# Kernel tuning notes

Measured on AMD Instinct MI355X. Metric: run time of the kernel, lower is better.

The kernel has to match this reference:

```python
import jax, jax.numpy as jnp
import numpy as np

H = 768          # hidden_size
NH = 12          # num_attention_heads
DH = H // NH     # attention_head_size = 64
NE_TYPES = 16    # num_edge_types
B, S = 4, 512
N = B * S        # flattened node count
E = 131072       # number of edges


def setup_inputs() -> dict:
    key = jax.random.key(0)
    ks = jax.random.split(key, 12)
    inp = {
        "hidden_states": jax.random.normal(ks[0], (B, S, H), dtype=jnp.float32),
        "Wq": jax.random.normal(ks[1], (H, H), dtype=jnp.float32) * 0.02,
        "bq": jnp.zeros((H,), dtype=jnp.float32),
        "Wk": jax.random.normal(ks[2], (H, H), dtype=jnp.float32) * 0.02,
        "bk": jnp.zeros((H,), dtype=jnp.float32),
        "Wv": jax.random.normal(ks[3], (H, H), dtype=jnp.float32) * 0.02,
        "bv": jnp.zeros((H,), dtype=jnp.float32),
        "rel_key_emb": jax.random.normal(ks[4], (NE_TYPES, DH), dtype=jnp.float32) * 0.02,
        "rel_val_emb": jax.random.normal(ks[5], (NE_TYPES, DH), dtype=jnp.float32) * 0.02,
        "edges_src": jax.random.randint(ks[6], (E,), 0, N, dtype=jnp.int32),
        "edges_tgt": jax.random.randint(ks[7], (E,), 0, N, dtype=jnp.int32),
        "edges_type": jax.random.randint(ks[8], (E,), 0, NE_TYPES, dtype=jnp.int32),
        "edges_pos": jax.random.randint(ks[9], (E,), 0, NE_TYPES, dtype=jnp.int32),
    }
    return inp


def reference(hidden_states, Wq, bq, Wk, bk, Wv, bv, rel_key_emb, rel_val_emb,
              edges_src, edges_tgt, edges_type, edges_pos):
    b, s, h = hidden_states.shape
    n = b * s
    hs = hidden_states.reshape(n, h)
    # Q/K/V projections, split into heads: [N, NH, DH]
    q = (hs @ Wq.T + bq).reshape(n, NH, DH)
    k = (hs @ Wk.T + bk).reshape(n, NH, DH)
    v = (hs @ Wv.T + bv).reshape(n, NH, DH)
    # Edge gather + relative key embedding (broadcast over heads)
    src_key = k[edges_src] + rel_key_emb[edges_pos][:, None, :]      # [E, NH, DH]
    tgt_query = q[edges_tgt]                                          # [E, NH, DH]
    # Unnormalized exp attention scores per edge per head: [E, NH]
    scores = jnp.exp(jnp.sum(tgt_query * src_key, axis=-1) / jnp.sqrt(jnp.float32(DH)))
    # Segment softmax normalization via scatter-add over target nodes
    denom = jax.ops.segment_sum(scores, edges_tgt, num_segments=n)    # [N, NH]
    attn = scores / denom[edges_tgt]                                  # [E, NH]
    # Reweighted per-edge values (the meaningful computed quantity)
    src_val = v[edges_src] + rel_val_emb[edges_pos][:, None, :]       # [E, NH, DH]
    weighted = src_val * attn[:, :, None]                             # [E, NH, DH]
    # NOTE: the original torch forward returns hidden_states unchanged
    # (the attention chain is dead code). We return the computed edge-weighted
    # values as the correctness target for the gather->exp->scatter-softmax chain.
    return weighted
```

## Files before the change

### kernel.cpp

```cpp
#include <hip/hip_runtime.h>
#include <hip/hip_bf16.h>

#define H 768
#define NH 12
#define DH 64
#define NNODES 2048
#define NEDGES 131072

typedef __bf16 bf16x8 __attribute__((ext_vector_type(8)));
typedef float floatx4 __attribute__((ext_vector_type(4)));

#define GLOAD_LDS16(gptr, ldsptr)                                                        \
  __builtin_amdgcn_global_load_lds((const __attribute__((address_space(1))) void*)(gptr), \
                                   (__attribute__((address_space(3))) void*)(ldsptr),     \
                                   16, 0, 0)

__device__ __forceinline__ unsigned short f2bf(float x) {
  union { __hip_bfloat16 h; unsigned short u; } cv;
  cv.h = __float2bfloat16(x);
  return cv.u;
}

__global__ __launch_bounds__(256)
void convert_kernel(const float* __restrict__ hs,
                    const float* __restrict__ Wq,
                    const float* __restrict__ Wk,
                    const float* __restrict__ Wv,
                    __hip_bfloat16* __restrict__ hsb,
                    __hip_bfloat16* __restrict__ wb,
                    float* __restrict__ denom) {
  int i = blockIdx.x * 256 + threadIdx.x;
  const int n_hs4 = NNODES * H / 4;
  const int n_w4  = H * H / 4;
  if (i < n_hs4) {
    float4 v = ((const float4*)hs)[i];
    ((ushort4*)hsb)[i] = make_ushort4(f2bf(v.x), f2bf(v.y), f2bf(v.z), f2bf(v.w));
    return;
  }
  int j = i - n_hs4;
  if (j < 3 * n_w4) {
    const float* src = (j < n_w4) ? Wq : (j < 2 * n_w4 ? Wk : Wv);
    float4 v = ((const float4*)src)[j % n_w4];
    ((ushort4*)wb)[j] = make_ushort4(f2bf(v.x), f2bf(v.y), f2bf(v.z), f2bf(v.w));
    return;
  }
  int z = j - 3 * n_w4;
  if (z < NNODES * NH / 4) {
    ((float4*)denom)[z] = make_float4(0.f, 0.f, 0.f, 0.f);
  }
}

__global__ __launch_bounds__(256)
void qkv_gemm(const __hip_bfloat16* __restrict__ A,
              const __hip_bfloat16* __restrict__ Wb,
              const float* __restrict__ b0,
              const float* __restrict__ b1,
              const float* __restrict__ b2,
              float* __restrict__ out) {
  __shared__ __hip_bfloat16 As[128][32];
  __shared__ __hip_bfloat16 Bs[128][32];

  const int t    = threadIdx.x;
  const int wave = t >> 6;
  const int lane = t & 63;
  const int bm   = blockIdx.x * 128;
  const int bn   = blockIdx.y * 128;
  const int mat  = blockIdx.z;

  const __hip_bfloat16* B = Wb + (size_t)mat * H * H;
  const float* bias = (mat == 0) ? b0 : ((mat == 1) ? b1 : b2);
  float* C = out + (size_t)mat * NNODES * H;

  const int wm = (wave & 1) * 64;
  const int wn = (wave >> 1) * 64;
  const int lr = lane & 15;
  const int lq = lane >> 4;

  floatx4 acc[4][4] = {};

  const int ar = t >> 2;
  const int ac = (t & 3) * 8;
  __hip_bfloat16* AsF = &As[0][0];
  __hip_bfloat16* BsF = &Bs[0][0];

  for (int kt = 0; kt < H; kt += 32) {
    GLOAD_LDS16(A + (size_t)(bm + ar) * H + kt + ac,      AsF + t * 8);
    GLOAD_LDS16(A + (size_t)(bm + 64 + ar) * H + kt + ac, AsF + 64 * 32 + t * 8);
    GLOAD_LDS16(B + (size_t)(bn + ar) * H + kt + ac,      BsF + t * 8);
    GLOAD_LDS16(B + (size_t)(bn + 64 + ar) * H + kt + ac, BsF + 64 * 32 + t * 8);
    __syncthreads();

    bf16x8 af[4], bfr[4];
#pragma unroll
    for (int i = 0; i < 4; i++)
      af[i] = *(const bf16x8*)&As[wm + i * 16 + lr][lq * 8];
#pragma unroll
    for (int i = 0; i < 4; i++)
      bfr[i] = *(const bf16x8*)&Bs[wn + i * 16 + lr][lq * 8];
#pragma unroll
    for (int mi = 0; mi < 4; mi++)
#pragma unroll
      for (int ni = 0; ni < 4; ni++)
        acc[mi][ni] = __builtin_amdgcn_mfma_f32_16x16x32_bf16(
            af[mi], bfr[ni], acc[mi][ni], 0, 0, 0);
    __syncthreads();
  }

#pragma unroll
  for (int ni = 0; ni < 4; ni++) {
    int col = bn + wn + ni * 16 + lr;
    float bv = bias[col];
#pragma unroll
    for (int mi = 0; mi < 4; mi++) {
#pragma unroll
      for (int r = 0; r < 4; r++) {
        int row = bm + wm + mi * 16 + lq * 4 + r;
        C[(size_t)row * H + col] = acc[mi][ni][r] + bv;
      }
    }
  }
}

__global__ __launch_bounds__(256)
void scores_kernel(const float* __restrict__ Q, const float* __restrict__ K,
                   const float* __restrict__ relk,
                   const int* __restrict__ esrc, const int* __restrict__ etgt,
                   const int* __restrict__ epos,
                   float* __restrict__ scores, float* __restrict__ denom) {
  const int wave = threadIdx.x >> 6;
  const int lane = threadIdx.x & 63;
  const int e = blockIdx.x * 4 + wave;
  const int src = esrc[e], tgt = etgt[e], pos = epos[e];
  const int g = lane >> 4;
  const int off = (lane & 15) * 4;

  const float4 r4 = *(const float4*)(relk + pos * DH + off);
  float s[3];
#pragma unroll
  for (int c = 0; c < 3; c++) {
    const float4 q4 = *(const float4*)(Q + (size_t)tgt * H + c * 256 + lane * 4);
    const float4 k4 = *(const float4*)(K + (size_t)src * H + c * 256 + lane * 4);
    s[c] = q4.x * (k4.x + r4.x) + q4.y * (k4.y + r4.y) +
           q4.z * (k4.z + r4.z) + q4.w * (k4.w + r4.w);
  }
#pragma unroll
  for (int m = 1; m < 16; m <<= 1) {
    s[0] += __shfl_xor(s[0], m);
    s[1] += __shfl_xor(s[1], m);
    s[2] += __shfl_xor(s[2], m);
  }
  if ((lane & 15) == 0) {
#pragma unroll
    for (int c = 0; c < 3; c++) {
      float sc = __expf(s[c] * 0.125f);
      int h = c * 4 + g;
      scores[(size_t)e * NH + h] = sc;
      atomicAdd(denom + (size_t)tgt * NH + h, sc);
    }
  }
}

__global__ __launch_bounds__(256)
void weighted_kernel(const float* __restrict__ V, const float* __restrict__ relv,
                     const int* __restrict__ esrc, const int* __restrict__ etgt,
                     const int* __restrict__ epos,
                     const float* __restrict__ scores,
                     const float* __restrict__ denom,
                     float* __restrict__ out) {
  const int wave = threadIdx.x >> 6;
  const int lane = threadIdx.x & 63;
  const int e = blockIdx.x * 4 + wave;
  const int src = esrc[e], tgt = etgt[e], pos = epos[e];
  const int g = lane >> 4;
  const int off = (lane & 15) * 4;

  const float4 r4 = *(const float4*)(relv + pos * DH + off);
#pragma unroll
  for (int c = 0; c < 3; c++) {
    int h = c * 4 + g;
    float a = scores[(size_t)e * NH + h] / denom[(size_t)tgt * NH + h];
    float4 v4 = *(const float4*)(V + (size_t)src * H + c * 256 + lane * 4);
    floatx4 o;
    o.x = (v4.x + r4.x) * a;
    o.y = (v4.y + r4.y) * a;
    o.z = (v4.z + r4.z) * a;
    o.w = (v4.w + r4.w) * a;
    __builtin_nontemporal_store(o, (floatx4*)(out + (size_t)e * H + c * 256 + lane * 4));
  }
}

extern "C" void kernel_launch(void* const* d_in, const int* in_sizes, int n_in,
                              void* d_out, int out_size, void* d_ws, size_t ws_size,
                              hipStream_t stream) {
  const float* hs   = (const float*)d_in[0];
  const float* Wq   = (const float*)d_in[1];
  const float* bq   = (const float*)d_in[2];
  const float* Wk   = (const float*)d_in[3];
  const float* bk   = (const float*)d_in[4];
  const float* Wv   = (const float*)d_in[5];
  const float* bv   = (const float*)d_in[6];
  const float* relk = (const float*)d_in[7];
  const float* relv = (const float*)d_in[8];
  const int* esrc   = (const int*)d_in[9];
  const int* etgt   = (const int*)d_in[10];
  const int* epos   = (const int*)d_in[12];
  float* out = (float*)d_out;

  char* ws = (char*)d_ws;
  __hip_bfloat16* hsb = (__hip_bfloat16*)ws;
  __hip_bfloat16* wb  = (__hip_bfloat16*)(ws + 3145728);
  float* qkv    = (float*)(ws + 6684672);
  float* scores = (float*)(ws + 25559040);
  float* denom  = (float*)(ws + 31850496);

  convert_kernel<<<3288, 256, 0, stream>>>(hs, Wq, Wk, Wv, hsb, wb, denom);

  dim3 grid_gemm(16, 6, 3);
  qkv_gemm<<<grid_gemm, 256, 0, stream>>>(hsb, wb, bq, bk, bv, qkv);

  const float* Qp = qkv;
  const float* Kp = qkv + (size_t)NNODES * H;
  const float* Vp = qkv + (size_t)2 * NNODES * H;

  scores_kernel<<<NEDGES / 4, 256, 0, stream>>>(Qp, Kp, relk, esrc, etgt, epos,
                                                scores, denom);

  weighted_kernel<<<NEDGES / 4, 256, 0, stream>>>(Vp, relv, esrc, etgt, epos,
                                                  scores, denom, out);
}
```

Before: 539.8 us.

## Compute dense per-head QK^T via bf16 MFMA and gather edge scores from it

Instead of gathering full Q and K rows per edge and reducing in a wave, this computes the full 2048x2048 score matrix per head with a bf16 MFMA GEMM. It also precomputes the Q·rel_key terms for all 16 positions. Edge scores then become two scalar gathers plus exp and an atomic add. This trades the per-edge gather traffic for writing and reading a ~200MB dense score matrix, and it lowers QK precision to bf16. It only runs when the workspace is large enough, otherwise the old path is used.

```diff
diff --git a/kernel.cpp b/kernel.cpp
--- a/kernel.cpp
+++ b/kernel.cpp
@@ -118,6 +118,127 @@
         C[(size_t)row * H + col] = acc[mi][ni][r] + bv;
       }
     }
+  }
+}
+
+__global__ __launch_bounds__(256)
+void repack_kernel(const float* __restrict__ Q, const float* __restrict__ K,
+                   __hip_bfloat16* __restrict__ Qh, __hip_bfloat16* __restrict__ Kh) {
+  int tid = blockIdx.x * 256 + threadIdx.x;
+  int d4 = tid & 15;
+  int th = tid >> 4;
+  int h  = th % NH;
+  int t  = th / NH;
+  size_t in_off  = (size_t)t * H + h * DH + d4 * 4;
+  size_t out_off = ((size_t)h * NNODES + t) * DH + d4 * 4;
+  float4 q4 = *(const float4*)(Q + in_off);
+  float4 k4 = *(const float4*)(K + in_off);
+  *(ushort4*)((unsigned short*)Qh + out_off) =
+      make_ushort4(f2bf(q4.x * 0.125f), f2bf(q4.y * 0.125f),
+                   f2bf(q4.z * 0.125f), f2bf(q4.w * 0.125f));
+  *(ushort4*)((unsigned short*)Kh + out_off) =
+      make_ushort4(f2bf(k4.x), f2bf(k4.y), f2bf(k4.z), f2bf(k4.w));
+}
+
+__global__ __launch_bounds__(256)
+void qrel_kernel(const float* __restrict__ Q, const float* __restrict__ relk,
+                 float* __restrict__ qrel) {
+  int t = blockIdx.x;
+  int tid = threadIdx.x;
+  if (tid >= 16 * NH) return;
+  int h = tid % NH;
+  int p = tid / NH;
+  const float* q = Q + (size_t)t * H + h * DH;
+  const float* r = relk + p * DH;
+  float s = 0.f;
+#pragma unroll 8
+  for (int d = 0; d < DH; d++) s += q[d] * r[d];
+  qrel[((size_t)t * 16 + p) * NH + h] = s * 0.125f;
+}
+
+__global__ __launch_bounds__(256)
+void sgemm_kernel(const __hip_bfloat16* __restrict__ Qh,
+                  const __hip_bfloat16* __restrict__ Kh,
+                  float* __restrict__ S) {
+  __shared__ __hip_bfloat16 As[128][32];
+  __shared__ __hip_bfloat16 Bs[128][32];
+
+  const int t    = threadIdx.x;
+  const int wave = t >> 6;
+  const int lane = t & 63;
+  const int bm   = blockIdx.x * 128;
+  const int bn   = blockIdx.y * 128;
+  const int h    = blockIdx.z;
+
+  const __hip_bfloat16* A = Qh + (size_t)h * NNODES * DH;
+  const __hip_bfloat16* B = Kh + (size_t)h * NNODES * DH;
+  float* C = S + (size_t)h * NNODES * NNODES;
+
+  const int wm = (wave & 1) * 64;
+  const int wn = (wave >> 1) * 64;
+  const int lr = lane & 15;
+  const int lq = lane >> 4;
+
+  floatx4 acc[4][4] = {};
+
+  const int ar = t >> 2;
+  const int ac = (t & 3) * 8;
+  __hip_bfloat16* AsF = &As[0][0];
+  __hip_bfloat16* BsF = &Bs[0][0];
+
+  for (int kt = 0; kt < DH; kt += 32) {
+    GLOAD_LDS16(A + (size_t)(bm + ar) * DH + kt + ac,      AsF + t * 8);
+    GLOAD_LDS16(A + (size_t)(bm + 64 + ar) * DH + kt + ac, AsF + 64 * 32 + t * 8);
+    GLOAD_LDS16(B + (size_t)(bn + ar) * DH + kt + ac,      BsF + t * 8);
+    GLOAD_LDS16(B + (size_t)(bn + 64 + ar) * DH + kt + ac, BsF + 64 * 32 + t * 8);
+    __syncthreads();
+
+    bf16x8 af[4], bfr[4];
+#pragma unroll
+    for (int i = 0; i < 4; i++)
+      af[i] = *(const bf16x8*)&As[wm + i * 16 + lr][lq * 8];
+#pragma unroll
+    for (int i = 0; i < 4; i++)
+      bfr[i] = *(const bf16x8*)&Bs[wn + i * 16 + lr][lq * 8];
+#pragma unroll
+    for (int mi = 0; mi < 4; mi++)
+#pragma unroll
+      for (int ni = 0; ni < 4; ni++)
+        acc[mi][ni] = __builtin_amdgcn_mfma_f32_16x16x32_bf16(
+            af[mi], bfr[ni], acc[mi][ni], 0, 0, 0);
+    __syncthreads();
+  }
+
+#pragma unroll
+  for (int ni = 0; ni < 4; ni++) {
+    int col = bn + wn + ni * 16 + lr;
+#pragma unroll
+    for (int mi = 0; mi < 4; mi++) {
+#pragma unroll
+      for (int r = 0; r < 4; r++) {
+        int row = bm + wm + mi * 16 + lq * 4 + r;
+        __builtin_nontemporal_store(acc[mi][ni][r],
+                                    C + (size_t)row * NNODES + col);
+      }
+    }
+  }
+}
+
+__global__ __launch_bounds__(256)
+void scores2_kernel(const float* __restrict__ S, const float* __restrict__ qrel,
+                    const int* __restrict__ esrc, const int* __restrict__ etgt,
+                    const int* __restrict__ epos,
+                    float* __restrict__ scores, float* __restrict__ denom) {
+  int tid = blockIdx.x * 256 + threadIdx.x;
+  int e = tid >> 4;
+  int h = tid & 15;
+  int src = esrc[e], tgt = etgt[e], pos = epos[e];
+  if (h < NH) {
+    float s = S[(size_t)h * NNODES * NNODES + (size_t)tgt * NNODES + src]
+            + qrel[((size_t)tgt * 16 + pos) * NH + h];
+    float sc = __expf(s);
+    scores[(size_t)e * NH + h] = sc;
+    atomicAdd(denom + (size_t)tgt * NH + h, sc);
   }
 }
 
@@ -212,6 +333,11 @@
   float* qkv    = (float*)(ws + 6684672);
   float* scores = (float*)(ws + 25559040);
   float* denom  = (float*)(ws + 31850496);
+  __hip_bfloat16* Qh = (__hip_bfloat16*)(ws + 31948800);
+  __hip_bfloat16* Kh = (__hip_bfloat16*)(ws + 35094528);
+  float* qrel   = (float*)(ws + 38240256);
+  float* Sm     = (float*)(ws + 39813120);
+  const size_t WS_NEED = 241139712ULL;
 
   convert_kernel<<<3288, 256, 0, stream>>>(hs, Wq, Wk, Wv, hsb, wb, denom);
 
@@ -222,8 +348,17 @@
   const float* Kp = qkv + (size_t)NNODES * H;
   const float* Vp = qkv + (size_t)2 * NNODES * H;
 
-  scores_kernel<<<NEDGES / 4, 256, 0, stream>>>(Qp, Kp, relk, esrc, etgt, epos,
-                                                scores, denom);
+  if (ws_size >= WS_NEED) {
+    repack_kernel<<<1536, 256, 0, stream>>>(Qp, Kp, Qh, Kh);
+    qrel_kernel<<<NNODES, 256, 0, stream>>>(Qp, relk, qrel);
+    dim3 grid_s(16, 16, NH);
+    sgemm_kernel<<<grid_s, 256, 0, stream>>>(Qh, Kh, Sm);
+    scores2_kernel<<<NEDGES * 16 / 256, 256, 0, stream>>>(Sm, qrel, esrc, etgt,
+                                                          epos, scores, denom);
+  } else {
+    scores_kernel<<<NEDGES / 4, 256, 0, stream>>>(Qp, Kp, relk, esrc, etgt, epos,
+                                                  scores, denom);
+  }
 
   weighted_kernel<<<NEDGES / 4, 256, 0, stream>>>(Vp, relv, esrc, etgt, epos,
                                                   scores, denom, out);
```

Measured after the change: 589.0 us. 9.1% more time.

## Sort edges by target into CSR and reduce softmax denominators per node

Applied to the files above, without the earlier changes.

The edges are now bucketed by target node. A histogram, a single-block scan and an atomic scatter build row pointers, permuted source and position arrays, and an inverse permutation. The scores kernel then runs one block per target node, keeps that node's Q row and the relative-key table in LDS, and sums the denominator inside the block instead of issuing a float atomicAdd per edge and head. The weighted kernel reads scores through the inverse permutation. This removes the contended float atomics and the repeated Q gathers, at the cost of three extra small launches, load imbalance across nodes of different degree, and an extra indirection.

```diff
diff --git a/kernel.cpp b/kernel.cpp
--- a/kernel.cpp
+++ b/kernel.cpp
@@ -28,7 +28,7 @@
                     const float* __restrict__ Wv,
                     __hip_bfloat16* __restrict__ hsb,
                     __hip_bfloat16* __restrict__ wb,
-                    float* __restrict__ denom) {
+                    int* __restrict__ hist) {
   int i = blockIdx.x * 256 + threadIdx.x;
   const int n_hs4 = NNODES * H / 4;
   const int n_w4  = H * H / 4;
@@ -45,8 +45,8 @@
     return;
   }
   int z = j - 3 * n_w4;
-  if (z < NNODES * NH / 4) {
-    ((float4*)denom)[z] = make_float4(0.f, 0.f, 0.f, 0.f);
+  if (z < NNODES / 4) {
+    ((int4*)hist)[z] = make_int4(0, 0, 0, 0);
   }
 }
 
@@ -122,41 +122,115 @@
 }
 
 __global__ __launch_bounds__(256)
-void scores_kernel(const float* __restrict__ Q, const float* __restrict__ K,
-                   const float* __restrict__ relk,
-                   const int* __restrict__ esrc, const int* __restrict__ etgt,
-                   const int* __restrict__ epos,
-                   float* __restrict__ scores, float* __restrict__ denom) {
-  const int wave = threadIdx.x >> 6;
-  const int lane = threadIdx.x & 63;
-  const int e = blockIdx.x * 4 + wave;
-  const int src = esrc[e], tgt = etgt[e], pos = epos[e];
-  const int g = lane >> 4;
-  const int off = (lane & 15) * 4;
-
-  const float4 r4 = *(const float4*)(relk + pos * DH + off);
-  float s[3];
-#pragma unroll
-  for (int c = 0; c < 3; c++) {
-    const float4 q4 = *(const float4*)(Q + (size_t)tgt * H + c * 256 + lane * 4);
-    const float4 k4 = *(const float4*)(K + (size_t)src * H + c * 256 + lane * 4);
-    s[c] = q4.x * (k4.x + r4.x) + q4.y * (k4.y + r4.y) +
-           q4.z * (k4.z + r4.z) + q4.w * (k4.w + r4.w);
-  }
-#pragma unroll
-  for (int m = 1; m < 16; m <<= 1) {
-    s[0] += __shfl_xor(s[0], m);
-    s[1] += __shfl_xor(s[1], m);
-    s[2] += __shfl_xor(s[2], m);
-  }
+void hist_kernel(const int* __restrict__ etgt, int* __restrict__ hist) {
+  int e = blockIdx.x * 256 + threadIdx.x;
+  atomicAdd(&hist[etgt[e]], 1);
+}
+
+__global__ __launch_bounds__(256)
+void scan_kernel(const int* __restrict__ hist, int* __restrict__ rowptr,
+                 int* __restrict__ cursor) {
+  __shared__ int part[256];
+  int t = threadIdx.x;
+  int loc[8];
+  int s = 0;
+#pragma unroll
+  for (int k = 0; k < 8; k++) { loc[k] = s; s += hist[t * 8 + k]; }
+  part[t] = s;
+  __syncthreads();
+  for (int off = 1; off < 256; off <<= 1) {
+    int v = (t >= off) ? part[t - off] : 0;
+    __syncthreads();
+    if (t >= off) part[t] += v;
+    __syncthreads();
+  }
+  int pre = part[t] - s;
+#pragma unroll
+  for (int k = 0; k < 8; k++) {
+    rowptr[t * 8 + k] = pre + loc[k];
+    cursor[t * 8 + k] = pre + loc[k];
+  }
+  if (t == 255) rowptr[NNODES] = part[255];
+}
+
+__global__ __launch_bounds__(256)
+void scatter_kernel(const int* __restrict__ esrc, const int* __restrict__ etgt,
+                    const int* __restrict__ epos,
+                    int* __restrict__ cursor,
+                    int* __restrict__ src_s, int* __restrict__ pos_s,
+                    int* __restrict__ einv) {
+  int e = blockIdx.x * 256 + threadIdx.x;
+  int tgt = etgt[e];
+  int slot = atomicAdd(&cursor[tgt], 1);
+  src_s[slot] = esrc[e];
+  pos_s[slot] = epos[e];
+  einv[e] = slot;
+}
+
+__global__ __launch_bounds__(256)
+void scores3_kernel(const float* __restrict__ Q, const float* __restrict__ K,
+                    const float* __restrict__ relk,
+                    const int* __restrict__ rowptr,
+                    const int* __restrict__ src_s, const int* __restrict__ pos_s,
+                    float* __restrict__ scores_s, float* __restrict__ denom) {
+  const int t    = blockIdx.x;
+  const int tid  = threadIdx.x;
+  const int wave = tid >> 6;
+  const int lane = tid & 63;
+  const int g    = lane >> 4;
+  const int off  = (lane & 15) * 4;
+
+  __shared__ float Qs[H];
+  __shared__ float Rk[16 * DH];
+  __shared__ float dpart[4][NH];
+
+  if (tid < 192)
+    *(float4*)&Qs[tid * 4] = *(const float4*)(Q + (size_t)t * H + tid * 4);
+  *(float4*)&Rk[tid * 4] = *(const float4*)(relk + tid * 4);
+  __syncthreads();
+
+  const int beg = rowptr[t], end = rowptr[t + 1];
+  float dacc0 = 0.f, dacc1 = 0.f, dacc2 = 0.f;
+
+  for (int i = beg + wave; i < end; i += 4) {
+    const int src = src_s[i];
+    const int pos = pos_s[i];
+    const float* Kp = K + (size_t)src * H;
+    const float4 r4 = *(const float4*)&Rk[pos * DH + off];
+    float s[3];
+#pragma unroll
+    for (int c = 0; c < 3; c++) {
+      float4 k4 = *(const float4*)(Kp + c * 256 + lane * 4);
+      float4 q4 = *(const float4*)&Qs[c * 256 + lane * 4];
+      s[c] = q4.x * (k4.x + r4.x) + q4.y * (k4.y + r4.y) +
+             q4.z * (k4.z + r4.z) + q4.w * (k4.w + r4.w);
+    }
+#pragma unroll
+    for (int m = 1; m < 16; m <<= 1) {
+      s[0] += __shfl_xor(s[0], m);
+      s[1] += __shfl_xor(s[1], m);
+      s[2] += __shfl_xor(s[2], m);
+    }
+    if ((lane & 15) == 0) {
+      float sc0 = __expf(s[0] * 0.125f);
+      float sc1 = __expf(s[1] * 0.125f);
+      float sc2 = __expf(s[2] * 0.125f);
+      scores_s[(size_t)i * NH + g]     = sc0;
+      scores_s[(size_t)i * NH + 4 + g] = sc1;
+      scores_s[(size_t)i * NH + 8 + g] = sc2;
+      dacc0 += sc0; dacc1 += sc1; dacc2 += sc2;
+    }
+  }
+
   if ((lane & 15) == 0) {
-#pragma unroll
-    for (int c = 0; c < 3; c++) {
-      float sc = __expf(s[c] * 0.125f);
-      int h = c * 4 + g;
-      scores[(size_t)e * NH + h] = sc;
-      atomicAdd(denom + (size_t)tgt * NH + h, sc);
-    }
+    dpart[wave][g]     = dacc0;
+    dpart[wave][4 + g] = dacc1;
+    dpart[wave][8 + g] = dacc2;
+  }
+  __syncthreads();
+  if (tid < NH) {
+    denom[(size_t)t * NH + tid] =
+        dpart[0][tid] + dpart[1][tid] + dpart[2][tid] + dpart[3][tid];
   }
 }
 
@@ -164,13 +238,15 @@
 void weighted_kernel(const float* __restrict__ V, const float* __restrict__ relv,
                      const int* __restrict__ esrc, const int* __restrict__ etgt,
                      const int* __restrict__ epos,
-                     const float* __restrict__ scores,
+                     const int* __restrict__ einv,
+                     const float* __restrict__ scores_s,
                      const float* __restrict__ denom,
                      float* __restrict__ out) {
   const int wave = threadIdx.x >> 6;
   const int lane = threadIdx.x & 63;
   const int e = blockIdx.x * 4 + wave;
   const int src = esrc[e], tgt = etgt[e], pos = epos[e];
+  const int sidx = einv[e];
   const int g = lane >> 4;
   const int off = (lane & 15) * 4;
 
@@ -178,7 +254,7 @@
 #pragma unroll
   for (int c = 0; c < 3; c++) {
     int h = c * 4 + g;
-    float a = scores[(size_t)e * NH + h] / denom[(size_t)tgt * NH + h];
+    float a = scores_s[(size_t)sidx * NH + h] / denom[(size_t)tgt * NH + h];
     float4 v4 = *(const float4*)(V + (size_t)src * H + c * 256 + lane * 4);
     floatx4 o;
     o.x = (v4.x + r4.x) * a;
@@ -209,11 +285,17 @@
   char* ws = (char*)d_ws;
   __hip_bfloat16* hsb = (__hip_bfloat16*)ws;
   __hip_bfloat16* wb  = (__hip_bfloat16*)(ws + 3145728);
-  float* qkv    = (float*)(ws + 6684672);
-  float* scores = (float*)(ws + 25559040);
-  float* denom  = (float*)(ws + 31850496);
-
-  convert_kernel<<<3288, 256, 0, stream>>>(hs, Wq, Wk, Wv, hsb, wb, denom);
+  float* qkv      = (float*)(ws + 6684672);
+  float* scores_s = (float*)(ws + 25559040);
+  float* denom    = (float*)(ws + 31850496);
+  int* hist       = (int*)(ws + 31948800);
+  int* rowptr     = (int*)(ws + 31956992);
+  int* cursor     = (int*)(ws + 31965200);
+  int* src_s = (int*)ws;
+  int* pos_s = (int*)(ws + 524288);
+  int* einv  = (int*)(ws + 1048576);
+
+  convert_kernel<<<3266, 256, 0, stream>>>(hs, Wq, Wk, Wv, hsb, wb, hist);
 
   dim3 grid_gemm(16, 6, 3);
   qkv_gemm<<<grid_gemm, 256, 0, stream>>>(hsb, wb, bq, bk, bv, qkv);
@@ -222,9 +304,14 @@
   const float* Kp = qkv + (size_t)NNODES * H;
   const float* Vp = qkv + (size_t)2 * NNODES * H;
 
-  scores_kernel<<<NEDGES / 4, 256, 0, stream>>>(Qp, Kp, relk, esrc, etgt, epos,
-                                                scores, denom);
+  hist_kernel<<<NEDGES / 256, 256, 0, stream>>>(etgt, hist);
+  scan_kernel<<<1, 256, 0, stream>>>(hist, rowptr, cursor);
+  scatter_kernel<<<NEDGES / 256, 256, 0, stream>>>(esrc, etgt, epos, cursor,
+                                                   src_s, pos_s, einv);
+
+  scores3_kernel<<<NNODES, 256, 0, stream>>>(Qp, Kp, relk, rowptr, src_s, pos_s,
+                                             scores_s, denom);
 
   weighted_kernel<<<NEDGES / 4, 256, 0, stream>>>(Vp, relv, esrc, etgt, epos,
-                                                  scores, denom, out);
-}
+                                                  einv, scores_s, denom, out);
+}
```

New measurement: 537.3 us. About the same (-0.5%).
